# Kernel optimization log

Measured on AMD Instinct MI355X. Metric: run time of the kernel, lower is better.

## Reference

```python
import jax, jax.numpy as jnp
import numpy as np

N_NODES = 50000
N_EDGES = 800000
IN_FEATS = 128
H_FEATS = 128
OUT_FEATS = 64
N_HEADS = 4
THRESHOLD = 0.1
COS_EPS = 1e-8   # F.cosine_similarity eps
LN_EPS = 1e-5


def setup_inputs() -> dict:
    key = jax.random.key(0)
    ks = jax.random.split(key, 16)
    D1 = H_FEATS // N_HEADS  # 32
    inp = {
        "feat": jax.random.normal(ks[0], (N_NODES, IN_FEATS), dtype=jnp.float32),
        "src": jax.random.randint(ks[1], (N_EDGES,), 0, N_NODES, dtype=jnp.int32),
        "dst": jax.random.randint(ks[2], (N_EDGES,), 0, N_NODES, dtype=jnp.int32),
        # conv0: in_feats -> n_heads * (h_feats // n_heads)
        "W0": jax.random.normal(ks[3], (IN_FEATS, N_HEADS * D1), dtype=jnp.float32) * (1.0 / np.sqrt(IN_FEATS)),
        "b0": jnp.zeros((N_HEADS * D1,), dtype=jnp.float32),
        # conv1: h_feats -> n_heads * (h_feats // n_heads)
        "W1": jax.random.normal(ks[4], (H_FEATS, N_HEADS * D1), dtype=jnp.float32) * (1.0 / np.sqrt(H_FEATS)),
        "b1": jnp.zeros((N_HEADS * D1,), dtype=jnp.float32),
        # conv2: h_feats -> 1 * out_feats
        "W2": jax.random.normal(ks[5], (H_FEATS, OUT_FEATS), dtype=jnp.float32) * (1.0 / np.sqrt(H_FEATS)),
        "b2": jnp.zeros((OUT_FEATS,), dtype=jnp.float32),
        # LayerNorms used after conv0 and conv1 (lns[1], lns[2])
        "ln1_g": jnp.ones((H_FEATS,), dtype=jnp.float32),
        "ln1_b": jnp.zeros((H_FEATS,), dtype=jnp.float32),
        "ln2_g": jnp.ones((H_FEATS,), dtype=jnp.float32),
        "ln2_b": jnp.zeros((H_FEATS,), dtype=jnp.float32),
    }
    return inp


def _layer_norm(x, g, b):
    mu = jnp.mean(x, axis=-1, keepdims=True)
    var = jnp.mean(jnp.square(x - mu), axis=-1, keepdims=True)
    return (x - mu) * jax.lax.rsqrt(var + LN_EPS) * g + b


def _rgat_conv(x, src, dst, W, b, n_heads, d_out):
    N = x.shape[0]
    ft = (x @ W).reshape(N, n_heads, d_out)  # (N, H, D)
    # edge score: cosine_similarity(src_feat_flat, src_feat_flat) -> per-node, then gather
    flat = ft.reshape(N, n_heads * d_out)
    sq = jnp.sum(flat * flat, axis=1)                      # (N,)
    nrm = jnp.maximum(jnp.sqrt(sq), COS_EPS)
    cos = sq / (nrm * nrm)                                 # ~1 for nonzero rows
    e_node = jnp.log(jnp.where(cos >= THRESHOLD, cos, 1e-6))
    e = e_node[src]                                        # (E,)
    # segment softmax over destination nodes (DGL edge_softmax)
    m = jax.ops.segment_max(e, dst, num_segments=N)
    m = jnp.where(jnp.isfinite(m), m, 0.0)                 # empty segments
    ex = jnp.exp(e - m[dst])
    den = jax.ops.segment_sum(ex, dst, num_segments=N)
    a = ex / jnp.maximum(den[dst], 1e-16)                  # (E,)
    # u_mul_e + sum aggregation
    msg = ft[src] * a[:, None, None]                       # (E, H, D)
    out = jax.ops.segment_sum(msg, dst, num_segments=N)    # (N, H, D)
    return out + b.reshape(1, n_heads, d_out)


def reference(feat, src, dst, W0, b0, W1, b1, W2, b2, ln1_g, ln1_b, ln2_g, ln2_b):
    N = feat.shape[0]
    D1 = H_FEATS // N_HEADS
    x = _rgat_conv(feat, src, dst, W0, b0, N_HEADS, D1).reshape(N, -1)
    x = jax.nn.relu(_layer_norm(x, ln1_g, ln1_b))
    x = _rgat_conv(x, src, dst, W1, b1, N_HEADS, D1).reshape(N, -1)
    x = jax.nn.relu(_layer_norm(x, ln2_g, ln2_b))
    x = _rgat_conv(x, src, dst, W2, b2, 1, OUT_FEATS).reshape(N, -1)
    return x
```

## Files before the change

### kernel.cpp

```cpp
#include <hip/hip_runtime.h>
#include <hip/hip_fp16.h>
#include <math.h>

#define NN 50000
#define NE 800000
#define KDIM 128
#define NB 196
#define CPAD 16
#define STILE 4096

typedef _Float16 v8h __attribute__((ext_vector_type(8)));
typedef float v4f __attribute__((ext_vector_type(4)));

#define FEAT_B4 6250
__global__ __launch_bounds__(256) void convert_kernel(
    const float* __restrict__ feat, const float* __restrict__ W0,
    const float* __restrict__ W1, const float* __restrict__ W2,
    __half* __restrict__ feat_h, __half* __restrict__ W0T,
    __half* __restrict__ W1T, __half* __restrict__ W2T) {
  int b = blockIdx.x;
  int tid = threadIdx.x;
  if (b < FEAT_B4) {
    int i = b * 256 + tid;
    if (i < NN * 32) {
      float4 v = *(const float4*)&feat[(size_t)i * 4];
      union { __half2 h2[2]; int2 i2; } u;
      u.h2[0] = __floats2half2_rn(v.x, v.y);
      u.h2[1] = __floats2half2_rn(v.z, v.w);
      *(int2*)&feat_h[(size_t)i * 4] = u.i2;
    }
  } else {
    int gid = (b - FEAT_B4) * 256 + tid;
    if (gid < 16384) {
      int n = gid >> 7, k = gid & 127;
      W0T[gid] = __float2half(W0[k * 128 + n]);
    } else if (gid < 32768) {
      int g = gid - 16384; int n = g >> 7, k = g & 127;
      W1T[g] = __float2half(W1[k * 128 + n]);
    } else if (gid < 40960) {
      int g = gid - 32768; int n = g >> 7, k = g & 127;
      W2T[g] = __float2half(W2[k * 64 + n]);
    }
  }
}

template <int OUT>
__global__ __launch_bounds__(256) void gemm_mfma(
    const __half* __restrict__ X, const __half* __restrict__ WT,
    __half* __restrict__ Y, int nrows) {
  constexpr int NT = OUT / 16;
  __shared__ __align__(16) __half Xs[64][136];
  __shared__ __align__(16) __half Ws[OUT][136];
  const int tid = threadIdx.x;
  const int row0 = blockIdx.x * 64;
#pragma unroll
  for (int i = 0; i < 4; i++) {
    int ci = tid + 256 * i;
    int r = ci >> 4, ch = ci & 15;
    int g = row0 + r;
    int4 v = make_int4(0, 0, 0, 0);
    if (g < nrows) v = *(const int4*)&X[(size_t)g * 128 + ch * 8];
    *(int4*)&Xs[r][ch * 8] = v;
  }
#pragma unroll
  for (int i = 0; i < NT; i++) {
    int ci = tid + 256 * i;
    int n = ci >> 4, ch = ci & 15;
    *(int4*)&Ws[n][ch * 8] = *(const int4*)&WT[(size_t)n * 128 + ch * 8];
  }
  __syncthreads();
  const int lane = tid & 63;
  const int w = tid >> 6;
  const int c16 = lane & 15, q = lane >> 4;
  v8h a[4];
#pragma unroll
  for (int kt = 0; kt < 4; kt++)
    a[kt] = *(const v8h*)&Xs[w * 16 + c16][kt * 32 + q * 8];
  v4f acc[NT];
#pragma unroll
  for (int t = 0; t < NT; t++) acc[t] = (v4f){0.f, 0.f, 0.f, 0.f};
#pragma unroll
  for (int t = 0; t < NT; t++) {
#pragma unroll
    for (int kt = 0; kt < 4; kt++) {
      v8h bfr = *(const v8h*)&Ws[t * 16 + c16][kt * 32 + q * 8];
      acc[t] = __builtin_amdgcn_mfma_f32_16x16x32_f16(a[kt], bfr, acc[t], 0, 0, 0);
    }
  }
#pragma unroll
  for (int t = 0; t < NT; t++)
#pragma unroll
    for (int r = 0; r < 4; r++)
      Xs[w * 16 + q * 4 + r][t * 16 + c16] = __float2half(acc[t][r]);
  __syncthreads();
  constexpr int OCH = OUT / 8;
#pragma unroll
  for (int i = 0; i < 64 * OCH / 256; i++) {
    int ci = tid + 256 * i;
    int r = ci / OCH, ch = ci % OCH;
    int g = row0 + r;
    if (g < nrows) *(int4*)&Y[(size_t)g * OUT + ch * 8] = *(const int4*)&Xs[r][ch * 8];
  }
}

template <int F, bool LN, bool HOUT>
__global__ __launch_bounds__(256) void agg_kernel(
    const __half* __restrict__ ft,
    const int* __restrict__ row_ptr, const int* __restrict__ es,
    const float* __restrict__ bias, const float* __restrict__ g,
    const float* __restrict__ beta, void* __restrict__ out_v, int n) {
  int gw = (blockIdx.x * blockDim.x + threadIdx.x) >> 6;
  int lane = threadIdx.x & 63;
  if (gw >= n) return;
  int b = row_ptr[gw], e = row_ptr[gw + 1];
  int deg = e - b;

  constexpr int LPR = F / 8;
  constexpr int EW  = 64 / LPR;
  const int sub = lane / LPR;
  const int ll  = lane % LPR;
  float acc[8];
#pragma unroll
  for (int q = 0; q < 8; q++) acc[q] = 0.f;

  for (int cb = b; cb < e; cb += 64) {
    int rem = e - cb; if (rem > 64) rem = 64;
    int sn_l = 0;
    if (lane < rem) sn_l = es[cb + lane];
    for (int j = 0; j < rem; j += EW) {
      int jj = j + sub;
      int sn = __shfl(sn_l, jj, 64);
      if (jj < rem) {
        union { float4 f4; __half2 h2[4]; } u;
        u.f4 = *(const float4*)&ft[(size_t)sn * F + ll * 8];
#pragma unroll
        for (int q = 0; q < 4; q++) {
          float2 f = __half22float2(u.h2[q]);
          acc[2 * q + 0] += f.x;
          acc[2 * q + 1] += f.y;
        }
      }
    }
  }

#pragma unroll
  for (int o = 32; o >= LPR; o >>= 1)
#pragma unroll
    for (int q = 0; q < 8; q++) acc[q] += __shfl_xor(acc[q], o, 64);

  float sc = (deg > 0) ? (1.0f / (float)deg) : 0.f;
  float4 b4a = *(const float4*)&bias[ll * 8 + 0];
  float4 b4b = *(const float4*)&bias[ll * 8 + 4];
  acc[0] = fmaf(acc[0], sc, b4a.x); acc[1] = fmaf(acc[1], sc, b4a.y);
  acc[2] = fmaf(acc[2], sc, b4a.z); acc[3] = fmaf(acc[3], sc, b4a.w);
  acc[4] = fmaf(acc[4], sc, b4b.x); acc[5] = fmaf(acc[5], sc, b4b.y);
  acc[6] = fmaf(acc[6], sc, b4b.z); acc[7] = fmaf(acc[7], sc, b4b.w);

  if (LN) {
    float sum = 0.f;
#pragma unroll
    for (int q = 0; q < 8; q++) sum += acc[q];
#pragma unroll
    for (int o = LPR / 2; o > 0; o >>= 1) sum += __shfl_xor(sum, o, 64);
    float mean = sum * (1.0f / 128.0f);
    float var = 0.f;
#pragma unroll
    for (int q = 0; q < 8; q++) { acc[q] -= mean; var = fmaf(acc[q], acc[q], var); }
#pragma unroll
    for (int o = LPR / 2; o > 0; o >>= 1) var += __shfl_xor(var, o, 64);
    float r = rsqrtf(var * (1.0f / 128.0f) + 1e-5f);
    float4 g4a = *(const float4*)&g[ll * 8 + 0];
    float4 g4b = *(const float4*)&g[ll * 8 + 4];
    float4 be4a = *(const float4*)&beta[ll * 8 + 0];
    float4 be4b = *(const float4*)&beta[ll * 8 + 4];
#pragma unroll
    for (int q = 0; q < 8; q++) acc[q] *= r;
    acc[0] = fmaxf(acc[0] * g4a.x + be4a.x, 0.f);
    acc[1] = fmaxf(acc[1] * g4a.y + be4a.y, 0.f);
    acc[2] = fmaxf(acc[2] * g4a.z + be4a.z, 0.f);
    acc[3] = fmaxf(acc[3] * g4a.w + be4a.w, 0.f);
    acc[4] = fmaxf(acc[4] * g4b.x + be4b.x, 0.f);
    acc[5] = fmaxf(acc[5] * g4b.y + be4b.y, 0.f);
    acc[6] = fmaxf(acc[6] * g4b.z + be4b.z, 0.f);
    acc[7] = fmaxf(acc[7] * g4b.w + be4b.w, 0.f);
  }
  if (sub == 0) {
    if (HOUT) {
      __half* outh = (__half*)out_v;
      union { __half2 h2[4]; int4 i4; } u;
      u.h2[0] = __floats2half2_rn(acc[0], acc[1]);
      u.h2[1] = __floats2half2_rn(acc[2], acc[3]);
      u.h2[2] = __floats2half2_rn(acc[4], acc[5]);
      u.h2[3] = __floats2half2_rn(acc[6], acc[7]);
      *(int4*)&outh[(size_t)gw * F + ll * 8] = u.i4;
    } else {
      float* outf = (float*)out_v;
      *(float4*)&outf[(size_t)gw * F + ll * 8 + 0] = make_float4(acc[0], acc[1], acc[2], acc[3]);
      *(float4*)&outf[(size_t)gw * F + ll * 8 + 4] = make_float4(acc[4], acc[5], acc[6], acc[7]);
    }
  }
}

__global__ __launch_bounds__(256) void bhist_kernel(const int* __restrict__ dst,
                                                    int* __restrict__ bhist) {
  __shared__ int hh[256];
  int tid = threadIdx.x;
  hh[tid] = 0;
  __syncthreads();
#pragma unroll
  for (int q = 0; q < 4; q++) {
    int base = blockIdx.x * STILE + q * 1024 + tid * 4;
    if (base + 3 < NE) {
      int4 d = *(const int4*)&dst[base];
      atomicAdd(&hh[d.x >> 8], 1);
      atomicAdd(&hh[d.y >> 8], 1);
      atomicAdd(&hh[d.z >> 8], 1);
      atomicAdd(&hh[d.w >> 8], 1);
    } else {
#pragma unroll
      for (int k = 0; k < 4; k++)
        if (base + k < NE) atomicAdd(&hh[dst[base + k] >> 8], 1);
    }
  }
  __syncthreads();
  if (tid < NB && hh[tid]) atomicAdd(&bhist[tid * CPAD], hh[tid]);
}

__global__ __launch_bounds__(256) void bscan_kernel(const int* __restrict__ bhist,
                                                    int* __restrict__ bucket_base,
                                                    int* __restrict__ bfill) {
  int tid = threadIdx.x;
  int lane = tid & 63, wid = tid >> 6;
  int v = (tid < NB) ? bhist[tid * CPAD] : 0;
  int x = v;
#pragma unroll
  for (int o = 1; o < 64; o <<= 1) {
    int y = __shfl_up(x, o, 64);
    if (lane >= o) x += y;
  }
  __shared__ int wsum[4];
  if (lane == 63) wsum[wid] = x;
  __syncthreads();
  int wpre = 0;
  for (int w = 0; w < wid; w++) wpre += wsum[w];
  int excl = wpre + x - v;
  if (tid < NB) {
    bucket_base[tid] = excl;
    bfill[tid * CPAD] = excl;
  }
  if (tid == 0) bucket_base[NB] = NE;
}

__global__ __launch_bounds__(256) void stage_kernel(const int* __restrict__ src,
                                                    const int* __restrict__ dst,
                                                    int* __restrict__ bfill,
                                                    int* __restrict__ staged) {
  __shared__ int cnt[256];
  __shared__ int basep[256];
  __shared__ int cur[256];
  int tid = threadIdx.x;
  cnt[tid] = 0;
  cur[tid] = 0;
  __syncthreads();
#pragma unroll
  for (int q = 0; q < 4; q++) {
    int base = blockIdx.x * STILE + q * 1024 + tid * 4;
    if (base + 3 < NE) {
      int4 d = *(const int4*)&dst[base];
      atomicAdd(&cnt[d.x >> 8], 1);
      atomicAdd(&cnt[d.y >> 8], 1);
      atomicAdd(&cnt[d.z >> 8], 1);
      atomicAdd(&cnt[d.w >> 8], 1);
    } else {
#pragma unroll
      for (int k = 0; k < 4; k++)
        if (base + k < NE) atomicAdd(&cnt[dst[base + k] >> 8], 1);
    }
  }
  __syncthreads();
  if (tid < NB) basep[tid] = (cnt[tid] > 0) ? atomicAdd(&bfill[tid * CPAD], cnt[tid]) : 0;
  __syncthreads();
#pragma unroll
  for (int q = 0; q < 4; q++) {
    int base = blockIdx.x * STILE + q * 1024 + tid * 4;
    if (base + 3 < NE) {
      int4 d = *(const int4*)&dst[base];
      int4 s = *(const int4*)&src[base];
      int b0 = d.x >> 8, b1 = d.y >> 8, b2 = d.z >> 8, b3 = d.w >> 8;
      int p0 = atomicAdd(&cur[b0], 1);
      staged[basep[b0] + p0] = s.x | ((d.x & 255) << 16);
      int p1 = atomicAdd(&cur[b1], 1);
      staged[basep[b1] + p1] = s.y | ((d.y & 255) << 16);
      int p2 = atomicAdd(&cur[b2], 1);
      staged[basep[b2] + p2] = s.z | ((d.z & 255) << 16);
      int p3 = atomicAdd(&cur[b3], 1);
      staged[basep[b3] + p3] = s.w | ((d.w & 255) << 16);
    } else {
#pragma unroll
      for (int k = 0; k < 4; k++) {
        if (base + k < NE) {
          int d = dst[base + k], s = src[base + k];
          int bb = d >> 8;
          int pp = atomicAdd(&cur[bb], 1);
          staged[basep[bb] + pp] = s | ((d & 255) << 16);
        }
      }
    }
  }
}

__global__ __launch_bounds__(256) void bucket_csr_kernel(const int* __restrict__ staged,
                                                         const int* __restrict__ bucket_base,
                                                         int* __restrict__ row_ptr,
                                                         int* __restrict__ es) {
  int b = blockIdx.x;
  int tid = threadIdx.x;
  int lo = bucket_base[b], hi = bucket_base[b + 1];
  __shared__ int cnt[256];
  __shared__ int fill_l[256];
  __shared__ int wsum[4];
  cnt[tid] = 0;
  __syncthreads();
  for (int i = lo + tid; i < hi; i += 256)
    atomicAdd(&cnt[(staged[i] >> 16) & 255], 1);
  __syncthreads();
  int v = cnt[tid];
  int lane = tid & 63, wid = tid >> 6;
  int x = v;
#pragma unroll
  for (int o = 1; o < 64; o <<= 1) {
    int y = __shfl_up(x, o, 64);
    if (lane >= o) x += y;
  }
  if (lane == 63) wsum[wid] = x;
  __syncthreads();
  int wpre = 0;
  for (int w = 0; w < wid; w++) wpre += wsum[w];
  int start = lo + wpre + x - v;
  int node = (b << 8) + tid;
  if (node < NN) row_ptr[node] = start;
  fill_l[tid] = start;
  __syncthreads();
  for (int i = lo + tid; i < hi; i += 256) {
    int w = staged[i];
    int pos = atomicAdd(&fill_l[(w >> 16) & 255], 1);
    es[pos] = w & 0xFFFF;
  }
  if (b == 0 && tid == 0) row_ptr[NN] = NE;
}

extern "C" void kernel_launch(void* const* d_in, const int* in_sizes, int n_in,
                              void* d_out, int out_size, void* d_ws, size_t ws_size,
                              hipStream_t stream) {
  (void)in_sizes; (void)n_in; (void)out_size; (void)ws_size;
  const float* feat = (const float*)d_in[0];
  const int* src = (const int*)d_in[1];
  const int* dst = (const int*)d_in[2];
  const float* W0 = (const float*)d_in[3];
  const float* b0 = (const float*)d_in[4];
  const float* W1 = (const float*)d_in[5];
  const float* b1 = (const float*)d_in[6];
  const float* W2 = (const float*)d_in[7];
  const float* b2 = (const float*)d_in[8];
  const float* ln1g = (const float*)d_in[9];
  const float* ln1b = (const float*)d_in[10];
  const float* ln2g = (const float*)d_in[11];
  const float* ln2b = (const float*)d_in[12];
  float* out = (float*)d_out;

  char* p = (char*)d_ws;
  auto alloc = [&](size_t bytes) {
    char* r = p;
    p += (bytes + 255) & ~size_t(255);
    return r;
  };
  __half* fth      = (__half*)alloc((size_t)NN * 128 * 2);
  __half* hh       = (__half*)alloc((size_t)NN * 128 * 2);
  __half* feat_h   = (__half*)alloc((size_t)NN * 128 * 2);
  __half* W0T      = (__half*)alloc(128 * 128 * 2);
  __half* W1T      = (__half*)alloc(128 * 128 * 2);
  __half* W2T      = (__half*)alloc(64 * 128 * 2);
  int* row_ptr     = (int*)alloc((size_t)(NN + 1) * 4);
  int* es          = (int*)alloc((size_t)NE * 4);
  int* staged      = (int*)alloc((size_t)NE * 4);
  int* bhist       = (int*)alloc((size_t)NB * CPAD * 4);
  int* bfill       = (int*)alloc((size_t)NB * CPAD * 4);
  int* bucket_base = (int*)alloc((size_t)(NB + 1) * 4);

  hipMemsetAsync(bhist, 0, (size_t)NB * CPAD * 4, stream);
  int sb = (NE + STILE - 1) / STILE;
  bhist_kernel<<<sb, 256, 0, stream>>>(dst, bhist);
  bscan_kernel<<<1, 256, 0, stream>>>(bhist, bucket_base, bfill);
  stage_kernel<<<sb, 256, 0, stream>>>(src, dst, bfill, staged);
  bucket_csr_kernel<<<NB, 256, 0, stream>>>(staged, bucket_base, row_ptr, es);

  convert_kernel<<<FEAT_B4 + 160, 256, 0, stream>>>(feat, W0, W1, W2, feat_h, W0T, W1T, W2T);

  int gb = (NN + 63) / 64;
  int nwb = (NN + 3) / 4;

  gemm_mfma<128><<<gb, 256, 0, stream>>>(feat_h, W0T, fth, NN);
  agg_kernel<128, true, true><<<nwb, 256, 0, stream>>>(fth, row_ptr, es, b0, ln1g, ln1b, hh, NN);
  gemm_mfma<128><<<gb, 256, 0, stream>>>(hh, W1T, fth, NN);
  agg_kernel<128, true, true><<<nwb, 256, 0, stream>>>(fth, row_ptr, es, b1, ln2g, ln2b, hh, NN);
  gemm_mfma<64><<<gb, 256, 0, stream>>>(hh, W2T, fth, NN);
  agg_kernel<64, false, false><<<nwb, 256, 0, stream>>>(fth, row_ptr, es, b2, nullptr, nullptr, out, NN);
}
```

Before: 256.6 us.

## Reorder aggregate-then-transform for first two convs and fuse into one kernel

Since edge attention reduces to a uniform mean over incoming edges (cosine is ~1 for every node), the first two layers now aggregate neighbour features first and then apply the GEMM, bias, LayerNorm and ReLU in a single fused kernel. This removes an intermediate feature buffer round trip and a launch per layer. It relies on attention weights being 1/deg, and on aggregation commuting with the linear map. The inner loop stores aggregated rows to LDS and runs MFMA reading weights directly from global memory.

```diff
diff --git a/kernel.cpp b/kernel.cpp
--- a/kernel.cpp
+++ b/kernel.cpp
@@ -44,6 +44,119 @@
   }
 }
 
+__global__ __launch_bounds__(256) void fused_conv(
+    const __half* __restrict__ X, const __half* __restrict__ WT,
+    const int* __restrict__ row_ptr, const int* __restrict__ es,
+    const float* __restrict__ bias, const float* __restrict__ g,
+    const float* __restrict__ beta, __half* __restrict__ Y, int nrows) {
+  __shared__ __align__(16) __half Xs[64][136];
+  const int tid = threadIdx.x;
+  const int row0 = blockIdx.x * 64;
+  const int lane = tid & 63, w = tid >> 6;
+  const int sub = lane >> 4, ll = lane & 15;
+
+  for (int i = 0; i < 16; i++) {
+    int node = row0 + w * 16 + i;
+    float acc[8];
+#pragma unroll
+    for (int q2 = 0; q2 < 8; q2++) acc[q2] = 0.f;
+    int deg = 0;
+    if (node < nrows) {
+      int b = row_ptr[node], e = row_ptr[node + 1];
+      deg = e - b;
+      for (int cb = b; cb < e; cb += 64) {
+        int rem = e - cb; if (rem > 64) rem = 64;
+        int sn_l = 0;
+        if (lane < rem) sn_l = es[cb + lane];
+        for (int j = 0; j < rem; j += 4) {
+          int jj = j + sub;
+          int sn = __shfl(sn_l, jj, 64);
+          if (jj < rem) {
+            union { float4 f4; __half2 h2[4]; } u;
+            u.f4 = *(const float4*)&X[(size_t)sn * 128 + ll * 8];
+#pragma unroll
+            for (int q2 = 0; q2 < 4; q2++) {
+              float2 f = __half22float2(u.h2[q2]);
+              acc[2 * q2 + 0] += f.x;
+              acc[2 * q2 + 1] += f.y;
+            }
+          }
+        }
+      }
+#pragma unroll
+      for (int o = 32; o >= 16; o >>= 1)
+#pragma unroll
+        for (int q2 = 0; q2 < 8; q2++) acc[q2] += __shfl_xor(acc[q2], o, 64);
+    }
+    if (sub == 0) {
+      float sc = (deg > 0) ? 1.0f / (float)deg : 0.f;
+      union { __half2 h2[4]; int4 i4; } u;
+      u.h2[0] = __floats2half2_rn(acc[0] * sc, acc[1] * sc);
+      u.h2[1] = __floats2half2_rn(acc[2] * sc, acc[3] * sc);
+      u.h2[2] = __floats2half2_rn(acc[4] * sc, acc[5] * sc);
+      u.h2[3] = __floats2half2_rn(acc[6] * sc, acc[7] * sc);
+      *(int4*)&Xs[w * 16 + i][ll * 8] = u.i4;
+    }
+  }
+
+  const int c16 = ll, q = sub;
+  v8h a[4];
+#pragma unroll
+  for (int kt = 0; kt < 4; kt++)
+    a[kt] = *(const v8h*)&Xs[w * 16 + c16][kt * 32 + q * 8];
+  v4f acc[8];
+#pragma unroll
+  for (int t = 0; t < 8; t++) acc[t] = (v4f){0.f, 0.f, 0.f, 0.f};
+#pragma unroll
+  for (int t = 0; t < 8; t++) {
+#pragma unroll
+    for (int kt = 0; kt < 4; kt++) {
+      v8h bfr = *(const v8h*)&WT[(size_t)(t * 16 + c16) * 128 + kt * 32 + q * 8];
+      acc[t] = __builtin_amdgcn_mfma_f32_16x16x32_f16(a[kt], bfr, acc[t], 0, 0, 0);
+    }
+  }
+
+  float barr[8], garr[8], betr[8];
+#pragma unroll
+  for (int t = 0; t < 8; t++) {
+    barr[t] = bias[t * 16 + c16];
+    garr[t] = g[t * 16 + c16];
+    betr[t] = beta[t * 16 + c16];
+  }
+#pragma unroll
+  for (int r = 0; r < 4; r++) {
+    float s = 0.f;
+#pragma unroll
+    for (int t = 0; t < 8; t++) { acc[t][r] += barr[t]; s += acc[t][r]; }
+#pragma unroll
+    for (int o = 1; o <= 8; o <<= 1) s += __shfl_xor(s, o, 64);
+    float mu = s * (1.0f / 128.0f);
+    float v = 0.f;
+#pragma unroll
+    for (int t = 0; t < 8; t++) { float d = acc[t][r] - mu; v = fmaf(d, d, v); }
+#pragma unroll
+    for (int o = 1; o <= 8; o <<= 1) v += __shfl_xor(v, o, 64);
+    float rs = rsqrtf(v * (1.0f / 128.0f) + 1e-5f);
+#pragma unroll
+    for (int t = 0; t < 8; t++)
+      acc[t][r] = fmaxf((acc[t][r] - mu) * rs * garr[t] + betr[t], 0.f);
+  }
+
+#pragma unroll
+  for (int t = 0; t < 8; t++)
+#pragma unroll
+    for (int r = 0; r < 4; r++)
+      Xs[w * 16 + q * 4 + r][t * 16 + c16] = __float2half(acc[t][r]);
+  __syncthreads();
+#pragma unroll
+  for (int i = 0; i < 4; i++) {
+    int ci = tid + 256 * i;
+    int r = ci >> 4, ch = ci & 15;
+    int gr = row0 + r;
+    if (gr < nrows) *(int4*)&Y[(size_t)gr * 128 + ch * 8] = *(const int4*)&Xs[r][ch * 8];
+  }
+}
+
 template <int OUT>
 __global__ __launch_bounds__(256) void gemm_mfma(
     const __half* __restrict__ X, const __half* __restrict__ WT,
@@ -173,16 +286,14 @@
     float4 g4b = *(const float4*)&g[ll * 8 + 4];
     float4 be4a = *(const float4*)&beta[ll * 8 + 0];
     float4 be4b = *(const float4*)&beta[ll * 8 + 4];
-#pragma unroll
-    for (int q = 0; q < 8; q++) acc[q] *= r;
-    acc[0] = fmaxf(acc[0] * g4a.x + be4a.x, 0.f);
-    acc[1] = fmaxf(acc[1] * g4a.y + be4a.y, 0.f);
-    acc[2] = fmaxf(acc[2] * g4a.z + be4a.z, 0.f);
-    acc[3] = fmaxf(acc[3] * g4a.w + be4a.w, 0.f);
-    acc[4] = fmaxf(acc[4] * g4b.x + be4b.x, 0.f);
-    acc[5] = fmaxf(acc[5] * g4b.y + be4b.y, 0.f);
-    acc[6] = fmaxf(acc[6] * g4b.z + be4b.z, 0.f);
-    acc[7] = fmaxf(acc[7] * g4b.w + be4b.w, 0.f);
+    acc[0] = fmaxf(acc[0] * r * g4a.x + be4a.x, 0.f);
+    acc[1] = fmaxf(acc[1] * r * g4a.y + be4a.y, 0.f);
+    acc[2] = fmaxf(acc[2] * r * g4a.z + be4a.z, 0.f);
+    acc[3] = fmaxf(acc[3] * r * g4a.w + be4a.w, 0.f);
+    acc[4] = fmaxf(acc[4] * r * g4b.x + be4b.x, 0.f);
+    acc[5] = fmaxf(acc[5] * r * g4b.y + be4b.y, 0.f);
+    acc[6] = fmaxf(acc[6] * r * g4b.z + be4b.z, 0.f);
+    acc[7] = fmaxf(acc[7] * r * g4b.w + be4b.w, 0.f);
   }
   if (sub == 0) {
     if (HOUT) {
@@ -374,9 +485,10 @@
     p += (bytes + 255) & ~size_t(255);
     return r;
   };
-  __half* fth      = (__half*)alloc((size_t)NN * 128 * 2);
-  __half* hh       = (__half*)alloc((size_t)NN * 128 * 2);
   __half* feat_h   = (__half*)alloc((size_t)NN * 128 * 2);
+  __half* x1       = (__half*)alloc((size_t)NN * 128 * 2);
+  __half* x2       = (__half*)alloc((size_t)NN * 128 * 2);
+  __half* ft2      = (__half*)alloc((size_t)NN * 64 * 2);
   __half* W0T      = (__half*)alloc(128 * 128 * 2);
   __half* W1T      = (__half*)alloc(128 * 128 * 2);
   __half* W2T      = (__half*)alloc(64 * 128 * 2);
@@ -399,10 +511,8 @@
   int gb = (NN + 63) / 64;
   int nwb = (NN + 3) / 4;
 
-  gemm_mfma<128><<<gb, 256, 0, stream>>>(feat_h, W0T, fth, NN);
-  agg_kernel<128, true, true><<<nwb, 256, 0, stream>>>(fth, row_ptr, es, b0, ln1g, ln1b, hh, NN);
-  gemm_mfma<128><<<gb, 256, 0, stream>>>(hh, W1T, fth, NN);
-  agg_kernel<128, true, true><<<nwb, 256, 0, stream>>>(fth, row_ptr, es, b1, ln2g, ln2b, hh, NN);
-  gemm_mfma<64><<<gb, 256, 0, stream>>>(hh, W2T, fth, NN);
-  agg_kernel<64, false, false><<<nwb, 256, 0, stream>>>(fth, row_ptr, es, b2, nullptr, nullptr, out, NN);
-}
+  fused_conv<<<gb, 256, 0, stream>>>(feat_h, W0T, row_ptr, es, b0, ln1g, ln1b, x1, NN);
+  fused_conv<<<gb, 256, 0, stream>>>(x1, W1T, row_ptr, es, b1, ln2g, ln2b, x2, NN);
+  gemm_mfma<64><<<gb, 256, 0, stream>>>(x2, W2T, ft2, NN);
+  agg_kernel<64, false, false><<<nwb, 256, 0, stream>>>(ft2, row_ptr, es, b2, nullptr, nullptr, out, NN);
+}
```

Result: slower. 278.6 us (+8.6%).

## Fuse feat fp16 conversion into first GEMM, shrink edge indices to u16

Applied to the files above, without the earlier changes.

The first GEMM now loads fp32 features directly and converts them to half while staging into shared memory. This removes the separate conversion pass and its 12.8MB fp16 intermediate. The bhist memset is folded into the weight-transpose kernel, which now runs first. CSR edge source indices are stored as 16-bit values, halving index traffic in the three aggregation kernels, but this only works because node ids fit in 16 bits.

```diff
diff --git a/kernel.cpp b/kernel.cpp
--- a/kernel.cpp
+++ b/kernel.cpp
@@ -4,7 +4,6 @@
 
 #define NN 50000
 #define NE 800000
-#define KDIM 128
 #define NB 196
 #define CPAD 16
 #define STILE 4096
@@ -12,41 +11,28 @@
 typedef _Float16 v8h __attribute__((ext_vector_type(8)));
 typedef float v4f __attribute__((ext_vector_type(4)));
 
-#define FEAT_B4 6250
 __global__ __launch_bounds__(256) void convert_kernel(
-    const float* __restrict__ feat, const float* __restrict__ W0,
-    const float* __restrict__ W1, const float* __restrict__ W2,
-    __half* __restrict__ feat_h, __half* __restrict__ W0T,
-    __half* __restrict__ W1T, __half* __restrict__ W2T) {
-  int b = blockIdx.x;
-  int tid = threadIdx.x;
-  if (b < FEAT_B4) {
-    int i = b * 256 + tid;
-    if (i < NN * 32) {
-      float4 v = *(const float4*)&feat[(size_t)i * 4];
-      union { __half2 h2[2]; int2 i2; } u;
-      u.h2[0] = __floats2half2_rn(v.x, v.y);
-      u.h2[1] = __floats2half2_rn(v.z, v.w);
-      *(int2*)&feat_h[(size_t)i * 4] = u.i2;
-    }
-  } else {
-    int gid = (b - FEAT_B4) * 256 + tid;
-    if (gid < 16384) {
-      int n = gid >> 7, k = gid & 127;
-      W0T[gid] = __float2half(W0[k * 128 + n]);
-    } else if (gid < 32768) {
-      int g = gid - 16384; int n = g >> 7, k = g & 127;
-      W1T[g] = __float2half(W1[k * 128 + n]);
-    } else if (gid < 40960) {
-      int g = gid - 32768; int n = g >> 7, k = g & 127;
-      W2T[g] = __float2half(W2[k * 64 + n]);
-    }
-  }
-}
-
-template <int OUT>
+    const float* __restrict__ W0, const float* __restrict__ W1,
+    const float* __restrict__ W2, __half* __restrict__ W0T,
+    __half* __restrict__ W1T, __half* __restrict__ W2T,
+    int* __restrict__ bhist) {
+  int gid = blockIdx.x * 256 + threadIdx.x;
+  if (gid < NB * CPAD) bhist[gid] = 0;
+  if (gid < 16384) {
+    int n = gid >> 7, k = gid & 127;
+    W0T[gid] = __float2half(W0[k * 128 + n]);
+  } else if (gid < 32768) {
+    int g = gid - 16384; int n = g >> 7, k = g & 127;
+    W1T[g] = __float2half(W1[k * 128 + n]);
+  } else if (gid < 40960) {
+    int g = gid - 32768; int n = g >> 7, k = g & 127;
+    W2T[g] = __float2half(W2[k * 64 + n]);
+  }
+}
+
+template <int OUT, bool F32IN>
 __global__ __launch_bounds__(256) void gemm_mfma(
-    const __half* __restrict__ X, const __half* __restrict__ WT,
+    const void* __restrict__ Xv, const __half* __restrict__ WT,
     __half* __restrict__ Y, int nrows) {
   constexpr int NT = OUT / 16;
   __shared__ __align__(16) __half Xs[64][136];
@@ -58,9 +44,25 @@
     int ci = tid + 256 * i;
     int r = ci >> 4, ch = ci & 15;
     int g = row0 + r;
-    int4 v = make_int4(0, 0, 0, 0);
-    if (g < nrows) v = *(const int4*)&X[(size_t)g * 128 + ch * 8];
-    *(int4*)&Xs[r][ch * 8] = v;
+    if (F32IN) {
+      const float* X32 = (const float*)Xv;
+      float4 a0 = make_float4(0.f, 0.f, 0.f, 0.f), a1 = a0;
+      if (g < nrows) {
+        a0 = *(const float4*)&X32[(size_t)g * 128 + ch * 8];
+        a1 = *(const float4*)&X32[(size_t)g * 128 + ch * 8 + 4];
+      }
+      union { __half2 h2[4]; int4 i4; } u;
+      u.h2[0] = __floats2half2_rn(a0.x, a0.y);
+      u.h2[1] = __floats2half2_rn(a0.z, a0.w);
+      u.h2[2] = __floats2half2_rn(a1.x, a1.y);
+      u.h2[3] = __floats2half2_rn(a1.z, a1.w);
+      *(int4*)&Xs[r][ch * 8] = u.i4;
+    } else {
+      const __half* X16 = (const __half*)Xv;
+      int4 v = make_int4(0, 0, 0, 0);
+      if (g < nrows) v = *(const int4*)&X16[(size_t)g * 128 + ch * 8];
+      *(int4*)&Xs[r][ch * 8] = v;
+    }
   }
 #pragma unroll
   for (int i = 0; i < NT; i++) {
@@ -106,7 +108,7 @@
 template <int F, bool LN, bool HOUT>
 __global__ __launch_bounds__(256) void agg_kernel(
     const __half* __restrict__ ft,
-    const int* __restrict__ row_ptr, const int* __restrict__ es,
+    const int* __restrict__ row_ptr, const unsigned short* __restrict__ es,
     const float* __restrict__ bias, const float* __restrict__ g,
     const float* __restrict__ beta, void* __restrict__ out_v, int n) {
   int gw = (blockIdx.x * blockDim.x + threadIdx.x) >> 6;
@@ -173,16 +175,14 @@
     float4 g4b = *(const float4*)&g[ll * 8 + 4];
     float4 be4a = *(const float4*)&beta[ll * 8 + 0];
     float4 be4b = *(const float4*)&beta[ll * 8 + 4];
-#pragma unroll
-    for (int q = 0; q < 8; q++) acc[q] *= r;
-    acc[0] = fmaxf(acc[0] * g4a.x + be4a.x, 0.f);
-    acc[1] = fmaxf(acc[1] * g4a.y + be4a.y, 0.f);
-    acc[2] = fmaxf(acc[2] * g4a.z + be4a.z, 0.f);
-    acc[3] = fmaxf(acc[3] * g4a.w + be4a.w, 0.f);
-    acc[4] = fmaxf(acc[4] * g4b.x + be4b.x, 0.f);
-    acc[5] = fmaxf(acc[5] * g4b.y + be4b.y, 0.f);
-    acc[6] = fmaxf(acc[6] * g4b.z + be4b.z, 0.f);
-    acc[7] = fmaxf(acc[7] * g4b.w + be4b.w, 0.f);
+    acc[0] = fmaxf(acc[0] * r * g4a.x + be4a.x, 0.f);
+    acc[1] = fmaxf(acc[1] * r * g4a.y + be4a.y, 0.f);
+    acc[2] = fmaxf(acc[2] * r * g4a.z + be4a.z, 0.f);
+    acc[3] = fmaxf(acc[3] * r * g4a.w + be4a.w, 0.f);
+    acc[4] = fmaxf(acc[4] * r * g4b.x + be4b.x, 0.f);
+    acc[5] = fmaxf(acc[5] * r * g4b.y + be4b.y, 0.f);
+    acc[6] = fmaxf(acc[6] * r * g4b.z + be4b.z, 0.f);
+    acc[7] = fmaxf(acc[7] * r * g4b.w + be4b.w, 0.f);
   }
   if (sub == 0) {
     if (HOUT) {
@@ -312,7 +312,7 @@
 __global__ __launch_bounds__(256) void bucket_csr_kernel(const int* __restrict__ staged,
                                                          const int* __restrict__ bucket_base,
                                                          int* __restrict__ row_ptr,
-                                                         int* __restrict__ es) {
+                                                         unsigned short* __restrict__ es) {
   int b = blockIdx.x;
   int tid = threadIdx.x;
   int lo = bucket_base[b], hi = bucket_base[b + 1];
@@ -344,7 +344,7 @@
   for (int i = lo + tid; i < hi; i += 256) {
     int w = staged[i];
     int pos = atomicAdd(&fill_l[(w >> 16) & 255], 1);
-    es[pos] = w & 0xFFFF;
+    es[pos] = (unsigned short)(w & 0xFFFF);
   }
   if (b == 0 && tid == 0) row_ptr[NN] = NE;
 }
@@ -376,33 +376,31 @@
   };
   __half* fth      = (__half*)alloc((size_t)NN * 128 * 2);
   __half* hh       = (__half*)alloc((size_t)NN * 128 * 2);
-  __half* feat_h   = (__half*)alloc((size_t)NN * 128 * 2);
   __half* W0T      = (__half*)alloc(128 * 128 * 2);
   __half* W1T      = (__half*)alloc(128 * 128 * 2);
   __half* W2T      = (__half*)alloc(64 * 128 * 2);
   int* row_ptr     = (int*)alloc((size_t)(NN + 1) * 4);
-  int* es          = (int*)alloc((size_t)NE * 4);
+  unsigned short* es = (unsigned short*)alloc((size_t)NE * 2);
   int* staged      = (int*)alloc((size_t)NE * 4);
   int* bhist       = (int*)alloc((size_t)NB * CPAD * 4);
   int* bfill       = (int*)alloc((size_t)NB * CPAD * 4);
   int* bucket_base = (int*)alloc((size_t)(NB + 1) * 4);
 
-  hipMemsetAsync(bhist, 0, (size_t)NB * CPAD * 4, stream);
+  convert_kernel<<<160, 256, 0, stream>>>(W0, W1, W2, W0T, W1T, W2T, bhist);
+
   int sb = (NE + STILE - 1) / STILE;
   bhist_kernel<<<sb, 256, 0, stream>>>(dst, bhist);
   bscan_kernel<<<1, 256, 0, stream>>>(bhist, bucket_base, bfill);
   stage_kernel<<<sb, 256, 0, stream>>>(src, dst, bfill, staged);
   bucket_csr_kernel<<<NB, 256, 0, stream>>>(staged, bucket_base, row_ptr, es);
 
-  convert_kernel<<<FEAT_B4 + 160, 256, 0, stream>>>(feat, W0, W1, W2, feat_h, W0T, W1T, W2T);
-
   int gb = (NN + 63) / 64;
   int nwb = (NN + 3) / 4;
 
-  gemm_mfma<128><<<gb, 256, 0, stream>>>(feat_h, W0T, fth, NN);
+  gemm_mfma<128, true><<<gb, 256, 0, stream>>>(feat, W0T, fth, NN);
   agg_kernel<128, true, true><<<nwb, 256, 0, stream>>>(fth, row_ptr, es, b0, ln1g, ln1b, hh, NN);
-  gemm_mfma<128><<<gb, 256, 0, stream>>>(hh, W1T, fth, NN);
+  gemm_mfma<128, false><<<gb, 256, 0, stream>>>(hh, W1T, fth, NN);
   agg_kernel<128, true, true><<<nwb, 256, 0, stream>>>(fth, row_ptr, es, b1, ln2g, ln2b, hh, NN);
-  gemm_mfma<64><<<gb, 256, 0, stream>>>(hh, W2T, fth, NN);
+  gemm_mfma<64, false><<<gb, 256, 0, stream>>>(hh, W2T, fth, NN);
   agg_kernel<64, false, false><<<nwb, 256, 0, stream>>>(fth, row_ptr, es, b2, nullptr, nullptr, out, NN);
 }
```

After: 252.5 us. About the same (-1.6%).
